# Performance work log

Hardware: AMD Instinct MI355X
Metric: run time of the kernel (lower is better)

Reference implementation:

```python
import jax, jax.numpy as jnp
import numpy as np

B, S, D, H = 4, 2048, 1024, 16
HD = D // H
SCALE = np.sqrt(HD).astype(np.float32)


def setup_inputs() -> dict:
    key = jax.random.key(0)
    ks = jax.random.split(key, 6)
    std = 1.0 / np.sqrt(D)
    return {
        "query": jax.random.normal(ks[0], (B, S, D), jnp.float32),
        "key": jax.random.normal(ks[1], (B, S, D), jnp.float32),
        "value": jax.random.normal(ks[2], (B, S, D), jnp.float32),
        "Wq": jax.random.normal(ks[3], (D, D), jnp.float32) * std,
        "bq": jnp.zeros((D,), jnp.float32),
        "Wk": jax.random.normal(ks[4], (D, D), jnp.float32) * std,
        "bk": jnp.zeros((D,), jnp.float32),
        "Wv": jax.random.normal(ks[5], (D, D), jnp.float32) * std,
        "bv": jnp.zeros((D,), jnp.float32),
    }


def _split_heads(x):
    # [B,S,D] -> [B,H,S,HD]
    return x.reshape(B, S, H, HD).transpose(0, 2, 1, 3)


def reference(query, key, value, Wq, bq, Wk, bk, Wv, bv):
    q = _split_heads(query @ Wq.T + bq)
    k = _split_heads(key @ Wk.T + bk)
    v = _split_heads(value @ Wv.T + bv)
    scores = jnp.einsum("bhqd,bhkd->bhqk", q, k) / SCALE
    attn = jax.nn.softmax(scores, axis=-1)  # dropout=0 (eval)
    ctx = jnp.einsum("bhqk,bhkd->bhqd", attn, v)
    return ctx.transpose(0, 2, 1, 3).reshape(B, S, D)
```

## Files before the change

### kernel.cpp

```cpp
#include <hip/hip_runtime.h>
#include <hip/hip_bf16.h>

typedef __attribute__((ext_vector_type(8))) short bf16x8;
typedef __attribute__((ext_vector_type(4))) float f32x4;
typedef __attribute__((ext_vector_type(16))) float f32x16;

#define SEQ 2048
#define DMODEL 1024
#define NH 16
#define HD 64
#define BATCH 4
#define BHTOT 64
#define BS 8192
#define QKV_ELEMS 8388608

#define C2EXP 0.1803368801111244f

__device__ __forceinline__ ushort f2bf(float f) {
  union { float f; unsigned u; } v; v.f = f;
  unsigned r = (v.u + 0x7FFFu + ((v.u >> 16) & 1u)) >> 16;
  return (ushort)r;
}

__device__ __forceinline__ unsigned pkbf(float a, float b) {
  union { __hip_bfloat162 h; unsigned u; } cv;
  cv.h = __float22bfloat162_rn(make_float2(a, b));
  return cv.u;
}

#if __has_builtin(__builtin_amdgcn_exp2f)
#define EXP2F(x) __builtin_amdgcn_exp2f(x)
#else
#define EXP2F(x) exp2f(x)
#endif

__global__ __launch_bounds__(256) void convert_w(
    const float* __restrict__ w0, const float* __restrict__ w1,
    const float* __restrict__ w2, ushort* __restrict__ out) {
  const float* src = blockIdx.y == 0 ? w0 : (blockIdx.y == 1 ? w1 : w2);
  size_t e = ((size_t)blockIdx.x * 256 + threadIdx.x) * 4;
  float4 v = *(const float4*)(src + e);
  ushort4 o = { f2bf(v.x), f2bf(v.y), f2bf(v.z), f2bf(v.w) };
  *(ushort4*)(out + (size_t)blockIdx.y * 1048576 + e) = o;
}

__global__ __launch_bounds__(256) void qkv_gemm(
    const float* __restrict__ x0, const float* __restrict__ x1, const float* __restrict__ x2,
    const ushort* __restrict__ Wb,
    const float* __restrict__ bq, const float* __restrict__ bk, const float* __restrict__ bv,
    ushort* __restrict__ qkv) {
  __shared__ ushort sA[128][40];
  __shared__ ushort sB[128][40];

  const int z = blockIdx.z;
  const float* X = z == 0 ? x0 : (z == 1 ? x1 : x2);
  const ushort* W = Wb + (size_t)z * 1048576;
  const float* bias = z == 0 ? bq : (z == 1 ? bk : bv);
  ushort* out = qkv + (size_t)z * QKV_ELEMS;

  const int t = threadIdx.x;
  const int m0 = blockIdx.x * 128;
  const int n0 = blockIdx.y * 128;
  const int w = t >> 6, l = t & 63, lr = l & 15, lhi = l >> 4;
  const int wr = (w >> 1) * 64, wc = (w & 1) * 64;

  f32x4 acc[4][4];
#pragma unroll
  for (int i = 0; i < 4; i++)
#pragma unroll
    for (int j = 0; j < 4; j++) acc[i][j] = (f32x4){0.f, 0.f, 0.f, 0.f};

  for (int k0 = 0; k0 < DMODEL; k0 += 32) {
#pragma unroll
    for (int i = 0; i < 4; i++) {
      int e = i * 256 + t;
      int row = e >> 3, col = (e & 7) * 4;
      float4 a = *(const float4*)(X + (size_t)(m0 + row) * DMODEL + k0 + col);
      ushort4 ab = { f2bf(a.x), f2bf(a.y), f2bf(a.z), f2bf(a.w) };
      *(ushort4*)(&sA[row][col]) = ab;
      ushort4 bb = *(const ushort4*)(W + (size_t)(n0 + row) * DMODEL + k0 + col);
      *(ushort4*)(&sB[row][col]) = bb;
    }
    __syncthreads();
    bf16x8 af[4], bfr[4];
#pragma unroll
    for (int mi = 0; mi < 4; mi++) af[mi] = *(const bf16x8*)(&sA[wr + mi * 16 + lr][lhi * 8]);
#pragma unroll
    for (int ni = 0; ni < 4; ni++) bfr[ni] = *(const bf16x8*)(&sB[wc + ni * 16 + lr][lhi * 8]);
#pragma unroll
    for (int mi = 0; mi < 4; mi++)
#pragma unroll
      for (int ni = 0; ni < 4; ni++)
        acc[mi][ni] = __builtin_amdgcn_mfma_f32_16x16x32_bf16(af[mi], bfr[ni], acc[mi][ni], 0, 0, 0);
    __syncthreads();
  }

#pragma unroll
  for (int mi = 0; mi < 4; mi++) {
#pragma unroll
    for (int ni = 0; ni < 4; ni++) {
      int col = n0 + wc + ni * 16 + lr;
      float bsv = bias[col];
      int h = col >> 6, hd = col & 63;
#pragma unroll
      for (int r = 0; r < 4; r++) {
        int row = m0 + wr + mi * 16 + lhi * 4 + r;
        int b = row >> 11, s = row & 2047;
        float vv = acc[mi][ni][r] + bsv;
        out[(((size_t)(b * NH + h)) * SEQ + s) * HD + hd] = f2bf(vv);
      }
    }
  }
}

__global__ __launch_bounds__(256) void attn_kernel(const ushort* __restrict__ qkv,
                                                   float* __restrict__ out) {
  __shared__ ushort Kt[2][64][72];
  __shared__ ushort Vt[2][64][72];

  const int rb = blockIdx.x;
  const int bid = (rb & 7) * 128 + (rb >> 3);
  const int bh = bid >> 4, qt = bid & 15;
  const int q0 = qt * 128;
  const int t = threadIdx.x, w = t >> 6, l = t & 63;
  const int lq = l & 31, hi = l >> 5, hi8 = hi * 8;

  const ushort* q = qkv;
  const ushort* k = qkv + QKV_ELEMS;
  const ushort* v = qkv + 2 * (size_t)QKV_ELEMS;
  const size_t base = (size_t)bh * SEQ * HD;

  const int krow = t >> 3, kcol = (t & 7) * 8;
  const int skv = t & 63;
  const int skvp = (skv & 51) | ((skv & 4) << 1) | ((skv & 8) >> 1);
  const int shb = (t >> 6) * 8;

  bf16x8 aq[4];
  {
    int qrow = q0 + w * 32 + lq;
#pragma unroll
    for (int ks = 0; ks < 4; ks++)
      aq[ks] = *(const bf16x8*)(q + base + (size_t)qrow * HD + ks * 16 + hi8);
  }

  float m2 = -1e30f, lsum = 0.f;
  f32x16 acc_o[2];
  acc_o[0] = (f32x16)(0.0f);
  acc_o[1] = (f32x16)(0.0f);

#pragma unroll
  for (int i = 0; i < 2; i++) {
    bf16x8 gk = *(const bf16x8*)(k + base + (size_t)(i * 32 + krow) * HD + kcol);
    *(bf16x8*)(&Kt[0][i * 32 + krow][kcol]) = gk;
    bf16x8 gv = *(const bf16x8*)(v + base + (size_t)skv * HD + shb + i * 32);
#pragma unroll
    for (int j = 0; j < 8; j++) Vt[0][shb + i * 32 + j][skvp] = ((ushort)gv[j]);
  }
  __syncthreads();

  for (int tile = 0; tile < SEQ / 64; tile++) {
    const int cur = tile & 1, nxt = cur ^ 1;
    const int kvn = ((tile + 1) & 31) * 64;

    bf16x8 gk[2], gv[2];
#pragma unroll
    for (int i = 0; i < 2; i++) {
      gk[i] = *(const bf16x8*)(k + base + (size_t)(kvn + i * 32 + krow) * HD + kcol);
      gv[i] = *(const bf16x8*)(v + base + (size_t)(kvn + skv) * HD + shb + i * 32);
    }

    f32x16 sc[2];
    sc[0] = (f32x16)(0.0f);
    sc[1] = (f32x16)(0.0f);
#pragma unroll
    for (int mt = 0; mt < 2; mt++)
#pragma unroll
      for (int ks = 0; ks < 4; ks++) {
        bf16x8 ak = *(const bf16x8*)(&Kt[cur][mt * 32 + lq][ks * 16 + hi8]);
        sc[mt] = __builtin_amdgcn_mfma_f32_32x32x16_bf16(ak, aq[ks], sc[mt], 0, 0, 0);
      }

    float tm = sc[0][0];
#pragma unroll
    for (int mt = 0; mt < 2; mt++)
#pragma unroll
      for (int r = 0; r < 16; r++) tm = fmaxf(tm, sc[mt][r]);
    tm *= C2EXP;
    tm = fmaxf(tm, __shfl_xor(tm, 32));
    if (__any(tm > m2 + 8.f)) {
      float mn = fmaxf(m2, tm);
      float alpha = EXP2F(m2 - mn);
      m2 = mn;
      lsum *= alpha;
#pragma unroll
      for (int r = 0; r < 16; r++) {
        int rowq = (r & 3) + 8 * (r >> 2) + 4 * hi;
        float ar = __shfl(alpha, (l & 32) | rowq);
        acc_o[0][r] *= ar;
        acc_o[1][r] *= ar;
      }
    }

    float rs = 0.f;
    unsigned c[2][8];
#pragma unroll
    for (int mt = 0; mt < 2; mt++)
#pragma unroll
      for (int i = 0; i < 8; i++) {
        float p0 = EXP2F(sc[mt][2 * i] * C2EXP - m2);
        float p1 = EXP2F(sc[mt][2 * i + 1] * C2EXP - m2);
        rs += p0 + p1;
        c[mt][i] = pkbf(p0, p1);
      }
    rs += __shfl_xor(rs, 32);
    lsum += rs;

#pragma unroll
    for (int s = 0; s < 4; s++) {
      union { unsigned u[4]; bf16x8 v8; } ap;
#pragma unroll
      for (int j = 0; j < 4; j++) ap.u[j] = c[s >> 1][(s & 1) * 4 + j];
#pragma unroll
      for (int nt = 0; nt < 2; nt++) {
        bf16x8 bv = *(const bf16x8*)(&Vt[cur][nt * 32 + lq][s * 16 + hi8]);
        acc_o[nt] = __builtin_amdgcn_mfma_f32_32x32x16_bf16(ap.v8, bv, acc_o[nt], 0, 0, 0);
      }
    }

#pragma unroll
    for (int i = 0; i < 2; i++) {
      *(bf16x8*)(&Kt[nxt][i * 32 + krow][kcol]) = gk[i];
#pragma unroll
      for (int j = 0; j < 8; j++) Vt[nxt][shb + i * 32 + j][skvp] = ((ushort)gv[i][j]);
    }
    __syncthreads();
  }

  const int b = bh >> 4, h = bh & 15;
  float inv = 1.f / lsum;
#pragma unroll
  for (int r = 0; r < 16; r++) {
    int rowq = (r & 3) + 8 * (r >> 2) + 4 * hi;
    float iv = __shfl(inv, (l & 32) | rowq);
    int s = q0 + w * 32 + rowq;
#pragma unroll
    for (int nt = 0; nt < 2; nt++)
      out[((size_t)(b * SEQ + s)) * DMODEL + h * HD + nt * 32 + lq] = acc_o[nt][r] * iv;
  }
}

extern "C" void kernel_launch(void* const* d_in, const int* in_sizes, int n_in,
                              void* d_out, int out_size, void* d_ws, size_t ws_size,
                              hipStream_t stream) {
  const float* query = (const float*)d_in[0];
  const float* key_  = (const float*)d_in[1];
  const float* value = (const float*)d_in[2];
  const float* Wq = (const float*)d_in[3];
  const float* bq = (const float*)d_in[4];
  const float* Wk = (const float*)d_in[5];
  const float* bk = (const float*)d_in[6];
  const float* Wv = (const float*)d_in[7];
  const float* bv = (const float*)d_in[8];

  ushort* Wb = (ushort*)d_ws;
  ushort* qkv = Wb + 3u * 1048576u;

  convert_w<<<dim3(1024, 3), 256, 0, stream>>>(Wq, Wk, Wv, Wb);
  qkv_gemm<<<dim3(64, 8, 3), 256, 0, stream>>>(query, key_, value, Wb, bq, bk, bv, qkv);
  attn_kernel<<<dim3(BHTOT * (SEQ / 128)), 256, 0, stream>>>(qkv, (float*)d_out);
}
```

Measured before the change: 232.7 us.

## Pre-convert activations to bf16 and load GEMM tiles via direct global-to-LDS

Adds a separate kernel that converts the fp32 query/key/value inputs to bf16 in workspace. A new QKV GEMM then loads bf16 tiles straight into LDS with global_load_lds, using an XOR swizzle in place of padding to avoid bank conflicts. This removes the in-loop fp32 load and convert work and the register staging from the GEMM main loop. In exchange it adds an extra full pass over the activations and depends on enough workspace, falling back to the old kernel otherwise.

```diff
diff --git a/kernel.cpp b/kernel.cpp
--- a/kernel.cpp
+++ b/kernel.cpp
@@ -34,6 +34,11 @@
 #define EXP2F(x) exp2f(x)
 #endif
 
+#define GLD16(gp, lp)                                                        \
+  __builtin_amdgcn_global_load_lds(                                          \
+      (const __attribute__((address_space(1))) void*)(gp),                   \
+      (__attribute__((address_space(3))) void*)(lp), 16, 0, 0)
+
 __global__ __launch_bounds__(256) void convert_w(
     const float* __restrict__ w0, const float* __restrict__ w1,
     const float* __restrict__ w2, ushort* __restrict__ out) {
@@ -44,7 +49,85 @@
   *(ushort4*)(out + (size_t)blockIdx.y * 1048576 + e) = o;
 }
 
-__global__ __launch_bounds__(256) void qkv_gemm(
+__global__ __launch_bounds__(256) void convert_x(
+    const float* __restrict__ x0, const float* __restrict__ x1,
+    const float* __restrict__ x2, ushort* __restrict__ out) {
+  const float* src = blockIdx.y == 0 ? x0 : (blockIdx.y == 1 ? x1 : x2);
+  size_t e = ((size_t)blockIdx.x * 256 + threadIdx.x) * 4;
+  float4 v = *(const float4*)(src + e);
+  ushort4 o = { f2bf(v.x), f2bf(v.y), f2bf(v.z), f2bf(v.w) };
+  *(ushort4*)(out + (size_t)blockIdx.y * (size_t)QKV_ELEMS + e) = o;
+}
+
+__global__ __launch_bounds__(256) void qkv_gemm_bf(
+    const ushort* __restrict__ Xb, const ushort* __restrict__ Wb,
+    const float* __restrict__ bq, const float* __restrict__ bk, const float* __restrict__ bv,
+    ushort* __restrict__ qkv) {
+  __shared__ ushort sA[128][32];
+  __shared__ ushort sB[128][32];
+
+  const int z = blockIdx.z;
+  const ushort* A = Xb + (size_t)z * QKV_ELEMS;
+  const ushort* W = Wb + (size_t)z * 1048576;
+  const float* bias = z == 0 ? bq : (z == 1 ? bk : bv);
+  ushort* out = qkv + (size_t)z * QKV_ELEMS;
+
+  const int t = threadIdx.x;
+  const int m0 = blockIdx.x * 128;
+  const int n0 = blockIdx.y * 128;
+  const int w = t >> 6, l = t & 63, lr = l & 15, lhi = l >> 4;
+  const int wr = (w >> 1) * 64, wc = (w & 1) * 64;
+
+  const int rl = l >> 2;
+  const int scol = ((l & 3) * 8) ^ ((rl & 3) << 3);
+  const int rcol = (lhi * 8) ^ ((lr & 3) << 3);
+
+  f32x4 acc[4][4];
+#pragma unroll
+  for (int i = 0; i < 4; i++)
+#pragma unroll
+    for (int j = 0; j < 4; j++) acc[i][j] = (f32x4){0.f, 0.f, 0.f, 0.f};
+
+  for (int k0 = 0; k0 < DMODEL; k0 += 32) {
+#pragma unroll
+    for (int i = 0; i < 2; i++) {
+      int c = w * 2 + i;
+      GLD16(A + (size_t)(m0 + c * 16 + rl) * DMODEL + k0 + scol, &sA[c * 16][0]);
+      GLD16(W + (size_t)(n0 + c * 16 + rl) * DMODEL + k0 + scol, &sB[c * 16][0]);
+    }
+    __syncthreads();
+    bf16x8 af[4], bfr[4];
+#pragma unroll
+    for (int mi = 0; mi < 4; mi++) af[mi] = *(const bf16x8*)(&sA[wr + mi * 16 + lr][rcol]);
+#pragma unroll
+    for (int ni = 0; ni < 4; ni++) bfr[ni] = *(const bf16x8*)(&sB[wc + ni * 16 + lr][rcol]);
+#pragma unroll
+    for (int mi = 0; mi < 4; mi++)
+#pragma unroll
+      for (int ni = 0; ni < 4; ni++)
+        acc[mi][ni] = __builtin_amdgcn_mfma_f32_16x16x32_bf16(af[mi], bfr[ni], acc[mi][ni], 0, 0, 0);
+    __syncthreads();
+  }
+
+#pragma unroll
+  for (int mi = 0; mi < 4; mi++) {
+#pragma unroll
+    for (int ni = 0; ni < 4; ni++) {
+      int col = n0 + wc + ni * 16 + lr;
+      float bsv = bias[col];
+      int h = col >> 6, hd = col & 63;
+#pragma unroll
+      for (int r = 0; r < 4; r++) {
+        int row = m0 + wr + mi * 16 + lhi * 4 + r;
+        int b = row >> 11, s = row & 2047;
+        float vv = acc[mi][ni][r] + bsv;
+        out[(((size_t)(b * NH + h)) * SEQ + s) * HD + hd] = f2bf(vv);
+      }
+    }
+  }
+}
+
+__global__ __launch_bounds__(256) void qkv_gemm_f32(
     const float* __restrict__ x0, const float* __restrict__ x1, const float* __restrict__ x2,
     const ushort* __restrict__ Wb,
     const float* __restrict__ bq, const float* __restrict__ bk, const float* __restrict__ bv,
@@ -264,8 +347,15 @@
 
   ushort* Wb = (ushort*)d_ws;
   ushort* qkv = Wb + 3u * 1048576u;
+  ushort* Xb = qkv + 3u * (size_t)QKV_ELEMS;
+  const size_t need = (3u * 1048576u + 6u * (size_t)QKV_ELEMS) * 2u;
 
   convert_w<<<dim3(1024, 3), 256, 0, stream>>>(Wq, Wk, Wv, Wb);
-  qkv_gemm<<<dim3(64, 8, 3), 256, 0, stream>>>(query, key_, value, Wb, bq, bk, bv, qkv);
+  if (ws_size >= need) {
+    convert_x<<<dim3(8192, 3), 256, 0, stream>>>(query, key_, value, Xb);
+    qkv_gemm_bf<<<dim3(64, 8, 3), 256, 0, stream>>>(Xb, Wb, bq, bk, bv, qkv);
+  } else {
+    qkv_gemm_f32<<<dim3(64, 8, 3), 256, 0, stream>>>(query, key_, value, Wb, bq, bk, bv, qkv);
+  }
   attn_kernel<<<dim3(BHTOT * (SEQ / 128)), 256, 0, stream>>>(qkv, (float*)d_out);
 }
```

Result: faster. 206.0 us (-11.5%).
